# Performance work log

Hardware: AMD Instinct MI355X
Metric: run time of the kernel (lower is better)

The kernel has to match this reference:

```python
import jax, jax.numpy as jnp
import numpy as np

N = 20000      # total nodes (1000 graphs x 20 nodes)
E = 160000     # total edges (avg degree 8)
B = 1000       # number of graphs
H = 2          # attention heads
C = 128        # out_channels per head (encoder_hidden)
D = H * C      # 256, node feature dim between layers
EMB = 64       # embed_dim / LSTM hidden
V = 5          # vocab
T = 21         # max_length decode steps
SOS = 1        # NT2IDX['U']
SQRT_C = float(np.sqrt(C))


def setup_inputs() -> dict:
    key = jax.random.key(0)
    ks = jax.random.split(key, 40)
    rn = lambda k, shape, s=0.05: (jax.random.normal(k, shape) * s).astype(jnp.float32)
    p = {}
    p['x'] = jax.random.normal(ks[0], (N, 4), jnp.float32)
    p['edge_index'] = jax.random.randint(ks[1], (2, E), 0, N)
    p['batch'] = jnp.repeat(jnp.arange(B), N // B)  # contiguous graph ids, all graphs nonempty
    p['gc_content'] = jax.random.uniform(ks[2], (B,), jnp.float32)
    p['seq_length'] = jnp.full((B,), 21.0, jnp.float32)
    # layer 0 TransformerConv (in=4 -> heads*C=256)
    p['c0_wq'] = rn(ks[3], (4, D)); p['c0_bq'] = rn(ks[4], (D,))
    p['c0_wk'] = rn(ks[5], (4, D)); p['c0_bk'] = rn(ks[6], (D,))
    p['c0_wv'] = rn(ks[7], (4, D)); p['c0_bv'] = rn(ks[8], (D,))
    p['c0_ws'] = rn(ks[9], (4, D)); p['c0_bs'] = rn(ks[10], (D,))
    # layers 1..2 stacked (in=256 -> 256)
    p['cw_q'] = rn(ks[11], (2, D, D)); p['cb_q'] = rn(ks[12], (2, D))
    p['cw_k'] = rn(ks[13], (2, D, D)); p['cb_k'] = rn(ks[14], (2, D))
    p['cw_v'] = rn(ks[15], (2, D, D)); p['cb_v'] = rn(ks[16], (2, D))
    p['cw_s'] = rn(ks[17], (2, D, D)); p['cb_s'] = rn(ks[18], (2, D))
    p['ln_g'] = jnp.ones((3, D), jnp.float32)
    p['ln_b'] = jnp.zeros((3, D), jnp.float32)
    p['enc_w'] = rn(ks[19], (D + 2, EMB)); p['enc_b'] = rn(ks[20], (EMB,))
    p['emb'] = rn(ks[21], (V, EMB), 1.0)
    p['w_ih'] = rn(ks[22], (EMB, 4 * EMB)); p['w_hh'] = rn(ks[23], (EMB, 4 * EMB))
    p['b_ih'] = rn(ks[24], (4 * EMB,)); p['b_hh'] = rn(ks[25], (4 * EMB,))
    p['fc_w'] = rn(ks[26], (EMB, V)); p['fc_b'] = rn(ks[27], (V,))
    return p


def _transformer_conv(x, src, tgt, wq, bq, wk, bk, wv, bv, ws, bs):
    # PyG TransformerConv, heads=H, concat=True, root_weight=True, no edge_attr.
    n = x.shape[0]
    q = (x @ wq + bq).reshape(n, H, C)[tgt]   # [E,H,C] query at target nodes
    k = (x @ wk + bk).reshape(n, H, C)[src]   # [E,H,C] key at source nodes
    v = (x @ wv + bv).reshape(n, H, C)[src]   # [E,H,C] value at source nodes
    score = (q * k).sum(-1) / SQRT_C          # [E,H]
    m = jax.ops.segment_max(score, tgt, num_segments=n)   # scatter-softmax (stable)
    a = jnp.exp(score - m[tgt])
    den = jax.ops.segment_sum(a, tgt, num_segments=n)
    alpha = a / den[tgt]                      # [E,H]
    out = jax.ops.segment_sum(alpha[..., None] * v, tgt, num_segments=n)  # [N,H,C]
    return out.reshape(n, D) + x @ ws + bs    # concat heads + skip (lin_skip)


def _layer_norm(x, g, b):
    mu = x.mean(-1, keepdims=True)
    var = ((x - mu) ** 2).mean(-1, keepdims=True)
    return (x - mu) * jax.lax.rsqrt(var + 1e-5) * g + b


def reference(x, edge_index, batch, gc_content, seq_length,
              c0_wq, c0_bq, c0_wk, c0_bk, c0_wv, c0_bv, c0_ws, c0_bs,
              cw_q, cb_q, cw_k, cb_k, cw_v, cb_v, cw_s, cb_s,
              ln_g, ln_b, enc_w, enc_b, emb, w_ih, w_hh, b_ih, b_hh, fc_w, fc_b):
    src, tgt = edge_index[0], edge_index[1]
    # ---- encoder: 3 TransformerConv + ReLU + LayerNorm (dropout=eval/identity) ----
    h = _transformer_conv(x, src, tgt, c0_wq, c0_bq, c0_wk, c0_bk, c0_wv, c0_bv, c0_ws, c0_bs)
    h = _layer_norm(jax.nn.relu(h), ln_g[0], ln_b[0])
    for i in range(2):
        h = _transformer_conv(h, src, tgt, cw_q[i], cb_q[i], cw_k[i], cb_k[i],
                              cw_v[i], cb_v[i], cw_s[i], cb_s[i])
        h = _layer_norm(jax.nn.relu(h), ln_g[i + 1], ln_b[i + 1])
    # ---- global mean pool per graph ----
    counts = jax.ops.segment_sum(jnp.ones((h.shape[0],), h.dtype), batch, num_segments=B)
    pool = jax.ops.segment_sum(h, batch, num_segments=B) / jnp.maximum(counts, 1.0)[:, None]
    gfeat = jnp.concatenate([pool, gc_content[:, None], seq_length[:, None]], axis=1)  # [B,258]
    enc = jax.nn.relu(gfeat @ enc_w + enc_b)  # [B,EMB]
    def step(carry, _):
        hs, cs, inp = carry
        g = inp @ w_ih + b_ih + hs @ w_hh + b_hh      # [B,4*EMB], torch gate order i,f,g,o
        i_g, f_g, g_g, o_g = jnp.split(g, 4, axis=-1)
        cs = jax.nn.sigmoid(f_g) * cs + jax.nn.sigmoid(i_g) * jnp.tanh(g_g)
        hs = jax.nn.sigmoid(o_g) * jnp.tanh(cs)
        logits = hs @ fc_w + fc_b                     # [B,V]
        tok = jnp.argmax(logits, axis=-1)
        return (hs, cs, emb[tok]), logits
    init = (enc, jnp.zeros_like(enc), jnp.broadcast_to(emb[SOS], (B, EMB)))
    _, logits = jax.lax.scan(step, init, None, length=T)  # [T,B,V]
    return jnp.transpose(logits, (1, 0, 2))               # [B,T,V]
```

## Files before the change

### kernel.cpp

```cpp
#include <hip/hip_runtime.h>
#include <math.h>

#define NN 20000
#define NNP 20096
#define NE 160000
#define NB 1000
#define EMB 64
#define NV 5
#define NT 21

typedef __attribute__((ext_vector_type(8))) short bf16x8;
typedef __attribute__((ext_vector_type(4))) float f32x4;

__device__ __forceinline__ float sigm(float x) { return 1.f / (1.f + expf(-x)); }

__device__ __forceinline__ ushort f2bf(float x) {
    unsigned u = __float_as_uint(x);
    unsigned r = (u + 0x7FFFu + ((u >> 16) & 1u)) >> 16;
    return (ushort)r;
}
__device__ __forceinline__ float bf2f(ushort h) {
    return __uint_as_float(((unsigned)h) << 16);
}

__device__ __forceinline__ void gl16(const ushort* g, ushort* l) {
    __builtin_amdgcn_global_load_lds((const __attribute__((address_space(1))) void*)g,
                                     (__attribute__((address_space(3))) void*)l, 16, 0, 0);
}

__global__ void k_fill(unsigned* p, int n, unsigned v) {
    int i = blockIdx.x * 256 + threadIdx.x;
    if (i < n) p[i] = v;
}

__global__ void k_count(const int* __restrict__ ei, int* __restrict__ deg,
                        int* __restrict__ bucket) {
    int e = blockIdx.x * 256 + threadIdx.x;
    if (e >= NE) return;
    int s = ei[e], t = ei[NE + e];
    int pos = atomicAdd(&deg[t], 1);
    if (pos < 64) bucket[(size_t)t * 64 + pos] = s;
}

__global__ void k_lin0(const float* __restrict__ x,
                       const float* __restrict__ wq, const float* __restrict__ bq,
                       const float* __restrict__ wk, const float* __restrict__ bk,
                       const float* __restrict__ wv, const float* __restrict__ bv,
                       const float* __restrict__ wss, const float* __restrict__ bss,
                       float* __restrict__ QV, ushort* __restrict__ Kb,
                       float* __restrict__ acc) {
    int idx = blockIdx.x * 256 + threadIdx.x;
    if (idx >= NN * 1024) return;
    int n = idx >> 10, j = idx & 1023;
    float x0 = x[n*4+0], x1 = x[n*4+1], x2 = x[n*4+2], x3 = x[n*4+3];
    const float* W; const float* bb; int col;
    if (j < 256)      { W = wq;  bb = bq;  col = j; }
    else if (j < 512) { W = wk;  bb = bk;  col = j - 256; }
    else if (j < 768) { W = wv;  bb = bv;  col = j - 512; }
    else              { W = wss; bb = bss; col = j - 768; }
    float v = bb[col] + x0*W[col] + x1*W[256+col] + x2*W[512+col] + x3*W[768+col];
    if (j < 256)      QV[(size_t)n*512 + col] = v;
    else if (j < 512) Kb[(size_t)n*256 + col] = f2bf(v);
    else if (j < 768) QV[(size_t)n*512 + 256 + col] = v;
    else              acc[(size_t)n*256 + col] = v;
}

__global__ void k_convW(const float* __restrict__ cwq, const float* __restrict__ cwk,
                        const float* __restrict__ cwv, const float* __restrict__ cws,
                        ushort* __restrict__ WtHT, ushort* __restrict__ WtLT) {
    int idx = blockIdx.x * 256 + threadIdx.x;
    if (idx >= 2 * 64 * 1024) return;
    int n = idx & 1023;
    int rest = idx >> 10;
    int kq = rest & 63;
    int l = rest >> 6;
    int wsel = n >> 8, col = n & 255;
    const float* W = (wsel == 0) ? cwq : (wsel == 1) ? cwk : (wsel == 2) ? cwv : cws;
    W += (size_t)l * 65536;
    ushort hv[4], lv[4];
    #pragma unroll
    for (int i = 0; i < 4; ++i) {
        float v = W[(size_t)(kq * 4 + i) * 256 + col];
        hv[i] = f2bf(v);
        lv[i] = f2bf(v - bf2f(hv[i]));
    }
    int k0 = kq * 4;
    int kt = k0 >> 5, c = (k0 >> 3) & 3, j0 = k0 & 7;
    size_t o = ((size_t)l * 32 * 1024 + (size_t)(kt * 4 + c) * 1024 + n) * 8 + j0;
    *(ushort4*)(WtHT + o) = make_ushort4(hv[0], hv[1], hv[2], hv[3]);
    *(ushort4*)(WtLT + o) = make_ushort4(lv[0], lv[1], lv[2], lv[3]);
}

__global__ __launch_bounds__(256, 3) void k_gemm4_mfma(
    const ushort* __restrict__ AhT, const ushort* __restrict__ AlT,
    const ushort* __restrict__ WtHT, const ushort* __restrict__ WtLT,
    const float* __restrict__ bq, const float* __restrict__ bk,
    const float* __restrict__ bv, const float* __restrict__ bs,
    float* __restrict__ QV, ushort* __restrict__ Kb,
    float* __restrict__ acc) {
    __shared__ __align__(16) ushort SB[2][2][4][128][8];

    int id = blockIdx.x;
    int xcd = id & 7;
    int q8 = id >> 3;
    int s8 = q8 >> 3;
    int cblk = q8 & 7;
    int rblk = xcd + 8 * s8;
    if (rblk >= 157) return;
    int row0 = rblk * 128;
    int wsel = cblk >> 1;
    int coll = (cblk & 1) * 128;
    const float* bias; float* C = nullptr; int ldc = 0; ushort* CK = nullptr;
    if (wsel == 0)      { bias = bq; C = QV;       ldc = 512; }
    else if (wsel == 1) { bias = bk; CK = Kb; }
    else if (wsel == 2) { bias = bv; C = QV + 256; ldc = 512; }
    else                { bias = bs; C = acc;      ldc = 256; }
    int ncol0 = cblk * 128;

    int tid = threadIdx.x;
    int w = tid >> 6, lane = tid & 63;
    int wr = w >> 1, wc = w & 1;
    int g = lane >> 4, r16 = lane & 15;

    int hl = w >> 1;
    const ushort* bsrc0 = (hl == 0) ? WtHT : WtLT;
    const ushort* bS[4];
    #pragma unroll
    for (int i = 0; i < 4; ++i) {
        int c = (w & 1) * 2 + (i >> 1);
        int half = i & 1;
        bS[i] = bsrc0 + ((size_t)c * 1024 + ncol0 + half * 64 + lane) * 8;
    }
    const size_t bstep = (size_t)4 * 1024 * 8;

    const ushort* aPH = AhT + ((size_t)g * NNP + row0 + wr * 64 + r16) * 8;
    const ushort* aPL = AlT + ((size_t)g * NNP + row0 + wr * 64 + r16) * 8;
    const size_t astep = (size_t)4 * NNP * 8;

    f32x4 accv[4][4];
    f32x4 zz = {0.f, 0.f, 0.f, 0.f};
    #pragma unroll
    for (int m = 0; m < 4; ++m)
        #pragma unroll
        for (int n = 0; n < 4; ++n) accv[m][n] = zz;

    auto stageB = [&](int buf) {
        #pragma unroll
        for (int i = 0; i < 4; ++i) {
            int c = (w & 1) * 2 + (i >> 1);
            int half = i & 1;
            gl16(bS[i], &SB[buf][hl][c][half * 64][0]);
            bS[i] += bstep;
        }
    };

    stageB(0);
    for (int kt = 0; kt < 8; ++kt) {
        int cur = kt & 1;
        bf16x8 aH[4], aL[4];
        #pragma unroll
        for (int m = 0; m < 4; ++m) {
            aH[m] = *(const bf16x8*)(aPH + m * 128);
            aL[m] = *(const bf16x8*)(aPL + m * 128);
        }
        aPH += astep; aPL += astep;
        if (kt < 7) {
            stageB(cur ^ 1);
            asm volatile("s_waitcnt vmcnt(12)" ::: "memory");
        } else {
            asm volatile("s_waitcnt vmcnt(8)" ::: "memory");
        }
        __builtin_amdgcn_sched_barrier(0);
        __builtin_amdgcn_s_barrier();

        bf16x8 bH[4], bL[4];
        #pragma unroll
        for (int n = 0; n < 4; ++n) {
            int rw = wc * 64 + n * 16 + r16;
            bH[n] = *(const bf16x8*)&SB[cur][0][g][rw][0];
            bL[n] = *(const bf16x8*)&SB[cur][1][g][rw][0];
        }
        #pragma unroll
        for (int m = 0; m < 4; ++m) {
            #pragma unroll
            for (int n = 0; n < 4; ++n) {
                accv[m][n] = __builtin_amdgcn_mfma_f32_16x16x32_bf16(aH[m], bH[n], accv[m][n], 0, 0, 0);
                accv[m][n] = __builtin_amdgcn_mfma_f32_16x16x32_bf16(aH[m], bL[n], accv[m][n], 0, 0, 0);
                accv[m][n] = __builtin_amdgcn_mfma_f32_16x16x32_bf16(aL[m], bH[n], accv[m][n], 0, 0, 0);
            }
        }
        __builtin_amdgcn_s_barrier();
    }

    float* sl = (float*)&SB[0][0][0][0][0] + w * 1088;
    int erow = lane >> 2;
    int ecb  = (lane & 3) * 16;
    #pragma unroll
    for (int m = 0; m < 4; ++m) {
        #pragma unroll
        for (int n = 0; n < 4; ++n) {
            int cl = coll + wc * 64 + n * 16 + r16;
            float bvv = bias[cl];
            #pragma unroll
            for (int r = 0; r < 4; ++r)
                sl[(g * 4 + r) * 68 + n * 16 + r16] = accv[m][n][r] + bvv;
        }
        int grow = row0 + wr * 64 + m * 16 + erow;
        if (grow < NN) {
            int ccol = coll + wc * 64 + ecb;
            if (CK) {
                unsigned p[8];
                #pragma unroll
                for (int i = 0; i < 8; ++i) {
                    unsigned lo = f2bf(sl[erow * 68 + ecb + 2 * i]);
                    unsigned hi = f2bf(sl[erow * 68 + ecb + 2 * i + 1]);
                    p[i] = lo | (hi << 16);
                }
                ushort* cp = CK + (size_t)grow * 256 + ccol;
                *(uint4*)cp = make_uint4(p[0], p[1], p[2], p[3]);
                *(uint4*)(cp + 8) = make_uint4(p[4], p[5], p[6], p[7]);
            } else {
                float4 v0 = *(float4*)&sl[erow * 68 + ecb + 0];
                float4 v1 = *(float4*)&sl[erow * 68 + ecb + 4];
                float4 v2 = *(float4*)&sl[erow * 68 + ecb + 8];
                float4 v3 = *(float4*)&sl[erow * 68 + ecb + 12];
                float* cp = C + (size_t)grow * ldc + ccol;
                ((float4*)cp)[0] = v0; ((float4*)cp)[1] = v1;
                ((float4*)cp)[2] = v2; ((float4*)cp)[3] = v3;
            }
        }
    }
}

__global__ __launch_bounds__(256) void k_attn_ln(const float* __restrict__ QV,
                                                 const ushort* __restrict__ Kb,
                                                 const int* __restrict__ deg,
                                                 const int* __restrict__ bucket,
                                                 const float* __restrict__ acc,
                                                 const float* __restrict__ lg,
                                                 const float* __restrict__ lb,
                                                 ushort* __restrict__ AhT,
                                                 ushort* __restrict__ AlT) {
    __shared__ float ssc[4][64];
    __shared__ int ssrc[4][64];
    __shared__ __align__(16) float srow[2][256];
    int ws = threadIdx.x >> 6, l = threadIdx.x & 63;
    int t = blockIdx.x * 2 + (ws >> 1);
    int h = ws & 1;
    int cnt = deg[t]; if (cnt > 64) cnt = 64;
    const int* bptr = bucket + (size_t)t * 64;
    int gq = l >> 4, pos = l & 15;
    const float* qp = QV + (size_t)t * 512 + h * 128 + pos * 8;
    float4 qa = *(const float4*)qp, qb = *(const float4*)(qp + 4);

    float m = -INFINITY, den = 0.f, o0 = 0.f, o1 = 0.f;
    for (int c0 = 0; c0 < cnt; c0 += 64) {
        int clen = cnt - c0; if (clen > 64) clen = 64;
        if (l < clen) ssrc[ws][l] = bptr[c0 + l];
        for (int e = gq; e < clen; e += 4) {
            int s = ssrc[ws][e];
            const ushort* kp = Kb + (size_t)s * 256 + h * 128 + pos * 8;
            uint4 kv = *(const uint4*)kp;
            float d = qa.x * __uint_as_float(kv.x << 16)
                    + qa.y * __uint_as_float(kv.x & 0xFFFF0000u)
                    + qa.z * __uint_as_float(kv.y << 16)
                    + qa.w * __uint_as_float(kv.y & 0xFFFF0000u)
                    + qb.x * __uint_as_float(kv.z << 16)
                    + qb.y * __uint_as_float(kv.z & 0xFFFF0000u)
                    + qb.z * __uint_as_float(kv.w << 16)
                    + qb.w * __uint_as_float(kv.w & 0xFFFF0000u);
            d += __shfl_xor(d, 1); d += __shfl_xor(d, 2);
            d += __shfl_xor(d, 4); d += __shfl_xor(d, 8);
            if (pos == 0) ssc[ws][e] = d * 0.08838834764831845f;
        }
        float sv = (l < clen) ? ssc[ws][l] : -INFINITY;
        float M = sv;
        #pragma unroll
        for (int off = 32; off; off >>= 1) M = fmaxf(M, __shfl_xor(M, off));
        float wl = (l < clen) ? expf(sv - M) : 0.f;
        float D = wl;
        #pragma unroll
        for (int off = 32; off; off >>= 1) D += __shfl_xor(D, off);
        ssc[ws][l] = wl;
        float nm = fmaxf(m, M);
        float so = expf(m - nm), sn = expf(M - nm);
        den = den * so + D * sn;
        o0 *= so; o1 *= so;
        float co0 = 0.f, co1 = 0.f;
        int p = 0;
        for (; p + 4 <= clen; p += 4) {
            float a0 = ssc[ws][p],     a1 = ssc[ws][p + 1];
            float a2 = ssc[ws][p + 2], a3 = ssc[ws][p + 3];
            int s0 = ssrc[ws][p],     s1 = ssrc[ws][p + 1];
            int s2 = ssrc[ws][p + 2], s3 = ssrc[ws][p + 3];
            float2 v0 = *(const float2*)(QV + (size_t)s0 * 512 + 256 + h * 128 + l * 2);
            float2 v1 = *(const float2*)(QV + (size_t)s1 * 512 + 256 + h * 128 + l * 2);
            float2 v2 = *(const float2*)(QV + (size_t)s2 * 512 + 256 + h * 128 + l * 2);
            float2 v3 = *(const float2*)(QV + (size_t)s3 * 512 + 256 + h * 128 + l * 2);
            co0 += a0 * v0.x + a1 * v1.x + a2 * v2.x + a3 * v3.x;
            co1 += a0 * v0.y + a1 * v1.y + a2 * v2.y + a3 * v3.y;
        }
        for (; p < clen; ++p) {
            float a = ssc[ws][p];
            int s = ssrc[ws][p];
            float2 v = *(const float2*)(QV + (size_t)s * 512 + 256 + h * 128 + l * 2);
            co0 += a * v.x; co1 += a * v.y;
        }
        o0 += co0 * sn; o1 += co1 * sn;
        m = nm;
    }
    float inv = (den > 0.f) ? 1.f / den : 0.f;
    float2 sk = *(const float2*)(acc + (size_t)t * 256 + h * 128 + l * 2);
    float v0 = fmaxf(sk.x + o0 * inv, 0.f);
    float v1 = fmaxf(sk.y + o1 * inv, 0.f);
    *(float2*)&srow[ws >> 1][h * 128 + l * 2] = make_float2(v0, v1);
    __syncthreads();
    if (ws < 2) {
        int tt = blockIdx.x * 2 + ws;
        float4 v = *(const float4*)&srow[ws][l * 4];
        float sum = v.x + v.y + v.z + v.w;
        #pragma unroll
        for (int o = 32; o; o >>= 1) sum += __shfl_xor(sum, o);
        float mu = sum * (1.f / 256.f);
        float d0 = v.x - mu, d1 = v.y - mu, d2 = v.z - mu, d3 = v.w - mu;
        float sq = d0*d0 + d1*d1 + d2*d2 + d3*d3;
        #pragma unroll
        for (int o = 32; o; o >>= 1) sq += __shfl_xor(sq, o);
        float rs = rsqrtf(sq * (1.f / 256.f) + 1e-5f);
        int d = l * 4;
        float4 gg = *(const float4*)(lg + d);
        float4 bb = *(const float4*)(lb + d);
        float e0 = d0 * rs * gg.x + bb.x;
        float e1 = d1 * rs * gg.y + bb.y;
        float e2 = d2 * rs * gg.z + bb.z;
        float e3 = d3 * rs * gg.w + bb.w;
        ushort4 hv, lv;
        hv.x = f2bf(e0); lv.x = f2bf(e0 - bf2f(hv.x));
        hv.y = f2bf(e1); lv.y = f2bf(e1 - bf2f(hv.y));
        hv.z = f2bf(e2); lv.z = f2bf(e2 - bf2f(hv.z));
        hv.w = f2bf(e3); lv.w = f2bf(e3 - bf2f(hv.w));
        size_t o = ((size_t)(l >> 1) * NNP + tt) * 8 + (l & 1) * 4;
        *(ushort4*)(AhT + o) = hv;
        *(ushort4*)(AlT + o) = lv;
    }
}

__global__ __launch_bounds__(64) void k_poolenc(const ushort* __restrict__ AhT,
                                                const ushort* __restrict__ AlT,
                                                const float* __restrict__ gc,
                                                const float* __restrict__ seq,
                                                const float* __restrict__ ew,
                                                const float* __restrict__ eb,
                                                float* __restrict__ hs) {
    int b = blockIdx.x, j = threadIdx.x;
    __shared__ __align__(16) float pool[256];
    int r = j >> 1, j0 = (j & 1) * 4;
    float4 s4 = make_float4(0.f, 0.f, 0.f, 0.f);
    for (int n = 0; n < 20; ++n) {
        size_t o = ((size_t)r * NNP + b * 20 + n) * 8 + j0;
        ushort4 hv = *(const ushort4*)(AhT + o);
        ushort4 lv = *(const ushort4*)(AlT + o);
        s4.x += bf2f(hv.x) + bf2f(lv.x);
        s4.y += bf2f(hv.y) + bf2f(lv.y);
        s4.z += bf2f(hv.z) + bf2f(lv.z);
        s4.w += bf2f(hv.w) + bf2f(lv.w);
    }
    const float inv20 = 1.f / 20.f;
    s4.x *= inv20; s4.y *= inv20; s4.z *= inv20; s4.w *= inv20;
    *(float4*)(&pool[j * 4]) = s4;
    __syncthreads();
    float sacc = eb[j];
    for (int k = 0; k < 256; ++k) sacc += pool[k] * ew[k * 64 + j];
    sacc += gc[b] * ew[256 * 64 + j] + seq[b] * ew[257 * 64 + j];
    hs[(size_t)b * 64 + j] = fmaxf(sacc, 0.f);
}

__global__ void k_xc(const float* __restrict__ emb, const float* __restrict__ wih,
                     float* __restrict__ xc) {
    int idx = blockIdx.x * 256 + threadIdx.x;
    if (idx >= 5 * 256) return;
    int v = idx >> 8, col = idx & 255;
    float s = 0.f;
    for (int k = 0; k < 64; ++k) s += emb[v * 64 + k] * wih[k * 256 + col];
    xc[idx] = s;
}

__global__ __launch_bounds__(64, 1) void k_decode(const float* __restrict__ whh,
                                                  const float* __restrict__ bih,
                                                  const float* __restrict__ bhh,
                                                  const float* __restrict__ xc,
                                                  const float* __restrict__ fcw,
                                                  const float* __restrict__ fcb,
                                                  const float* __restrict__ hs0,
                                                  float* __restrict__ out) {
    int b = blockIdx.x;
    int j = threadIdx.x;

    float wgt[4][64];
    #pragma unroll
    for (int k = 0; k < 64; ++k) {
        #pragma unroll
        for (int g = 0; g < 4; ++g)
            wgt[g][k] = whh[k * 256 + g * 64 + j];
    }
    float bs0 = bih[0 * 64 + j] + bhh[0 * 64 + j];
    float bs1 = bih[1 * 64 + j] + bhh[1 * 64 + j];
    float bs2 = bih[2 * 64 + j] + bhh[2 * 64 + j];
    float bs3 = bih[3 * 64 + j] + bhh[3 * 64 + j];
    float xcg[5][4];
    #pragma unroll
    for (int v = 0; v < 5; ++v)
        #pragma unroll
        for (int g = 0; g < 4; ++g) xcg[v][g] = xc[v * 256 + g * 64 + j];
    float fw0 = fcw[j * 5 + 0], fw1 = fcw[j * 5 + 1], fw2 = fcw[j * 5 + 2],
          fw3 = fcw[j * 5 + 3], fw4 = fcw[j * 5 + 4];
    float fb0 = fcb[0], fb1 = fcb[1], fb2 = fcb[2], fb3 = fcb[3], fb4 = fcb[4];

    float hj = hs0[(size_t)b * 64 + j];
    float cj = 0.f;
    int tok = 1;

    for (int t = 0; t < NT; ++t) {
        float xg0, xg1, xg2, xg3;
        if (tok == 0)      { xg0 = xcg[0][0]; xg1 = xcg[0][1]; xg2 = xcg[0][2]; xg3 = xcg[0][3]; }
        else if (tok == 1) { xg0 = xcg[1][0]; xg1 = xcg[1][1]; xg2 = xcg[1][2]; xg3 = xcg[1][3]; }
        else if (tok == 2) { xg0 = xcg[2][0]; xg1 = xcg[2][1]; xg2 = xcg[2][2]; xg3 = xcg[2][3]; }
        else if (tok == 3) { xg0 = xcg[3][0]; xg1 = xcg[3][1]; xg2 = xcg[3][2]; xg3 = xcg[3][3]; }
        else               { xg0 = xcg[4][0]; xg1 = xcg[4][1]; xg2 = xcg[4][2]; xg3 = xcg[4][3]; }
        float aA0 = 0.f, aA1 = 0.f, aA2 = 0.f, aA3 = 0.f;
        float aB0 = 0.f, aB1 = 0.f, aB2 = 0.f, aB3 = 0.f;
        #pragma unroll
        for (int k = 0; k < 64; k += 2) {
            float h0 = __uint_as_float(__builtin_amdgcn_readlane(__float_as_uint(hj), k));
            float h1 = __uint_as_float(__builtin_amdgcn_readlane(__float_as_uint(hj), k + 1));
            aA0 += h0 * wgt[0][k]; aA1 += h0 * wgt[1][k];
            aA2 += h0 * wgt[2][k]; aA3 += h0 * wgt[3][k];
            aB0 += h1 * wgt[0][k + 1]; aB1 += h1 * wgt[1][k + 1];
            aB2 += h1 * wgt[2][k + 1]; aB3 += h1 * wgt[3][k + 1];
        }
        float ig = sigm(bs0 + xg0 + (aA0 + aB0));
        float fg = sigm(bs1 + xg1 + (aA1 + aB1));
        float gt = tanhf(bs2 + xg2 + (aA2 + aB2));
        float og = sigm(bs3 + xg3 + (aA3 + aB3));
        cj = fg * cj + ig * gt;
        hj = og * tanhf(cj);
        float l0 = hj * fw0, l1 = hj * fw1, l2 = hj * fw2, l3 = hj * fw3, l4 = hj * fw4;
        #pragma unroll
        for (int off = 32; off; off >>= 1) {
            l0 += __shfl_xor(l0, off); l1 += __shfl_xor(l1, off);
            l2 += __shfl_xor(l2, off); l3 += __shfl_xor(l3, off);
            l4 += __shfl_xor(l4, off);
        }
        l0 += fb0; l1 += fb1; l2 += fb2; l3 += fb3; l4 += fb4;
        int tk = 0; float bv = l0;
        if (l1 > bv) { bv = l1; tk = 1; }
        if (l2 > bv) { bv = l2; tk = 2; }
        if (l3 > bv) { bv = l3; tk = 3; }
        if (l4 > bv) { bv = l4; tk = 4; }
        tok = tk;
        if (j < 5) {
            float myl = (j == 0) ? l0 : (j == 1) ? l1 : (j == 2) ? l2 : (j == 3) ? l3 : l4;
            out[(size_t)b * (NT * NV) + t * NV + j] = myl;
        }
    }
}

extern "C" void kernel_launch(void* const* d_in, const int* in_sizes, int n_in,
                              void* d_out, int out_size, void* d_ws, size_t ws_size,
                              hipStream_t stream) {
    const float* x    = (const float*)d_in[0];
    const int*   ei   = (const int*)d_in[1];
    const float* gc   = (const float*)d_in[3];
    const float* seq  = (const float*)d_in[4];
    const float* c0wq = (const float*)d_in[5];  const float* c0bq = (const float*)d_in[6];
    const float* c0wk = (const float*)d_in[7];  const float* c0bk = (const float*)d_in[8];
    const float* c0wv = (const float*)d_in[9];  const float* c0bv = (const float*)d_in[10];
    const float* c0ws = (const float*)d_in[11]; const float* c0bs = (const float*)d_in[12];
    const float* cwq  = (const float*)d_in[13]; const float* cbq  = (const float*)d_in[14];
    const float* cwk  = (const float*)d_in[15]; const float* cbk  = (const float*)d_in[16];
    const float* cwv  = (const float*)d_in[17]; const float* cbv  = (const float*)d_in[18];
    const float* cws  = (const float*)d_in[19]; const float* cbs  = (const float*)d_in[20];
    const float* lng  = (const float*)d_in[21]; const float* lnb  = (const float*)d_in[22];
    const float* ew   = (const float*)d_in[23]; const float* eb   = (const float*)d_in[24];
    const float* emb  = (const float*)d_in[25];
    const float* wih  = (const float*)d_in[26]; const float* whh  = (const float*)d_in[27];
    const float* bih  = (const float*)d_in[28]; const float* bhh  = (const float*)d_in[29];
    const float* fcw  = (const float*)d_in[30]; const float* fcb  = (const float*)d_in[31];
    (void)in_sizes; (void)n_in; (void)out_size; (void)ws_size;

    float* wsf  = (float*)d_ws;
    float* QV   = wsf;
    float* acc  = QV + (size_t)NN * 512;
    ushort* Kb  = (ushort*)(acc + (size_t)NN * 256);
    ushort* AhT = Kb + (size_t)NN * 256;
    ushort* AlT = AhT + (size_t)32 * NNP * 8;
    ushort* WtHT = AlT + (size_t)32 * NNP * 8;
    ushort* WtLT = WtHT + 2 * 32 * 1024 * 8;
    float* xc   = (float*)(WtLT + 2 * 32 * 1024 * 8);
    float* hs   = xc + 5 * 256;
    int* deg    = (int*)(hs + (size_t)NB * 64);
    int* bucket = deg + NN;

    k_fill<<<(NN + 255) / 256, 256, 0, stream>>>((unsigned*)deg, NN, 0u);
    k_count<<<(NE + 255) / 256, 256, 0, stream>>>(ei, deg, bucket);
    k_convW<<<512, 256, 0, stream>>>(cwq, cwk, cwv, cws, WtHT, WtLT);
    k_xc<<<5, 256, 0, stream>>>(emb, wih, xc);

    for (int L = 0; L < 3; ++L) {
        if (L == 0) {
            k_lin0<<<NN * 1024 / 256, 256, 0, stream>>>(x, c0wq, c0bq, c0wk, c0bk,
                                                        c0wv, c0bv, c0ws, c0bs, QV, Kb, acc);
        } else {
            int i = L - 1;
            k_gemm4_mfma<<<1280, 256, 0, stream>>>(AhT, AlT,
                WtHT + (size_t)i * 32 * 1024 * 8, WtLT + (size_t)i * 32 * 1024 * 8,
                cbq + i * 256, cbk + i * 256, cbv + i * 256, cbs + i * 256,
                QV, Kb, acc);
        }
        k_attn_ln<<<NN / 2, 256, 0, stream>>>(QV, Kb, deg, bucket, acc,
                                              lng + L * 256, lnb + L * 256, AhT, AlT);
    }
    k_poolenc<<<NB, 64, 0, stream>>>(AhT, AlT, gc, seq, ew, eb, hs);
    k_decode<<<NB, 64, 0, stream>>>(whh, bih, bhh, xc, fcw, fcb, hs, (float*)d_out);
}
```

Baseline: 345.9 us.

## Double-buffer A-operand register loads in MFMA GEMM and fully unroll K loop

Restructures the projection GEMM main loop so the global loads of A fragments for the next K tile are issued before the MFMAs for the current tile, using two register sets, and unrolls the loop by two with fixed LDS buffer indices. The aim is to hide global-load latency for A behind matrix-core work. The extra register sets raise register pressure, so launch bounds are lowered from 3 to 2 blocks per SM, which cuts occupancy. The vmcnt waits are retuned for the new order of loads.

Result: no change. 349.3 us (+1.0%).

```diff
diff --git a/kernel.cpp b/kernel.cpp
--- a/kernel.cpp
+++ b/kernel.cpp
@@ -91,7 +91,37 @@
     *(ushort4*)(WtLT + o) = make_ushort4(lv[0], lv[1], lv[2], lv[3]);
 }
 
-__global__ __launch_bounds__(256, 3) void k_gemm4_mfma(
+#define LOADA(SH, SL)                                        \
+    do {                                                     \
+        _Pragma("unroll")                                    \
+        for (int m_ = 0; m_ < 4; ++m_) {                     \
+            SH[m_] = *(const bf16x8*)(aPH + m_ * 128);       \
+            SL[m_] = *(const bf16x8*)(aPL + m_ * 128);       \
+        }                                                    \
+        aPH += astep; aPL += astep;                          \
+    } while (0)
+
+#define DOMFMA(BUF, SH, SL)                                                                       \
+    do {                                                                                          \
+        bf16x8 bH_[4], bL_[4];                                                                    \
+        _Pragma("unroll")                                                                         \
+        for (int n_ = 0; n_ < 4; ++n_) {                                                          \
+            int rw_ = wc * 64 + n_ * 16 + r16;                                                    \
+            bH_[n_] = *(const bf16x8*)&SB[BUF][0][g][rw_][0];                                     \
+            bL_[n_] = *(const bf16x8*)&SB[BUF][1][g][rw_][0];                                     \
+        }                                                                                         \
+        _Pragma("unroll")                                                                         \
+        for (int m_ = 0; m_ < 4; ++m_) {                                                          \
+            _Pragma("unroll")                                                                     \
+            for (int n_ = 0; n_ < 4; ++n_) {                                                      \
+                accv[m_][n_] = __builtin_amdgcn_mfma_f32_16x16x32_bf16(SH[m_], bH_[n_], accv[m_][n_], 0, 0, 0); \
+                accv[m_][n_] = __builtin_amdgcn_mfma_f32_16x16x32_bf16(SH[m_], bL_[n_], accv[m_][n_], 0, 0, 0); \
+                accv[m_][n_] = __builtin_amdgcn_mfma_f32_16x16x32_bf16(SL[m_], bH_[n_], accv[m_][n_], 0, 0, 0); \
+            }                                                                                     \
+        }                                                                                         \
+    } while (0)
+
+__global__ __launch_bounds__(256, 2) void k_gemm4_mfma(
     const ushort* __restrict__ AhT, const ushort* __restrict__ AlT,
     const ushort* __restrict__ WtHT, const ushort* __restrict__ WtLT,
     const float* __restrict__ bq, const float* __restrict__ bk,
@@ -154,41 +184,29 @@
         }
     };
 
+    bf16x8 aH0[4], aL0[4], aH1[4], aL1[4];
+    LOADA(aH0, aL0);
     stageB(0);
-    for (int kt = 0; kt < 8; ++kt) {
-        int cur = kt & 1;
-        bf16x8 aH[4], aL[4];
-        #pragma unroll
-        for (int m = 0; m < 4; ++m) {
-            aH[m] = *(const bf16x8*)(aPH + m * 128);
-            aL[m] = *(const bf16x8*)(aPL + m * 128);
-        }
-        aPH += astep; aPL += astep;
-        if (kt < 7) {
-            stageB(cur ^ 1);
+
+    #pragma unroll
+    for (int kk = 0; kk < 4; ++kk) {
+        LOADA(aH1, aL1);
+        stageB(1);
+        asm volatile("s_waitcnt vmcnt(12)" ::: "memory");
+        __builtin_amdgcn_sched_barrier(0);
+        __builtin_amdgcn_s_barrier();
+        DOMFMA(0, aH0, aL0);
+        __builtin_amdgcn_s_barrier();
+        if (kk < 3) {
+            LOADA(aH0, aL0);
+            stageB(0);
             asm volatile("s_waitcnt vmcnt(12)" ::: "memory");
         } else {
-            asm volatile("s_waitcnt vmcnt(8)" ::: "memory");
+            asm volatile("s_waitcnt vmcnt(0)" ::: "memory");
         }
         __builtin_amdgcn_sched_barrier(0);
         __builtin_amdgcn_s_barrier();
-
-        bf16x8 bH[4], bL[4];
-        #pragma unroll
-        for (int n = 0; n < 4; ++n) {
-            int rw = wc * 64 + n * 16 + r16;
-            bH[n] = *(const bf16x8*)&SB[cur][0][g][rw][0];
-            bL[n] = *(const bf16x8*)&SB[cur][1][g][rw][0];
-        }
-        #pragma unroll
-        for (int m = 0; m < 4; ++m) {
-            #pragma unroll
-            for (int n = 0; n < 4; ++n) {
-                accv[m][n] = __builtin_amdgcn_mfma_f32_16x16x32_bf16(aH[m], bH[n], accv[m][n], 0, 0, 0);
-                accv[m][n] = __builtin_amdgcn_mfma_f32_16x16x32_bf16(aH[m], bL[n], accv[m][n], 0, 0, 0);
-                accv[m][n] = __builtin_amdgcn_mfma_f32_16x16x32_bf16(aL[m], bH[n], accv[m][n], 0, 0, 0);
-            }
-        }
+        DOMFMA(1, aH1, aL1);
         __builtin_amdgcn_s_barrier();
     }
 
```
